# Kernel tuning notes

Hardware: AMD Instinct MI355X
Metric: run time of the kernel (lower is better)

Reference implementation:

```python
import jax, jax.numpy as jnp
import numpy as np

NUM_CLASSES = 10
BIN_STEP = 0.1
N_SAMPLES = 2_000_000
NUM_BINS = 10  # len(arange(0,1.1,0.1)) - 1


def setup_inputs() -> dict:
    key = jax.random.key(0)
    k1, k2 = jax.random.split(key)
    # scaled logits -> softmax so that all confidence bins (incl. (0.9,1.0]) are populated
    logits = jax.random.normal(k1, (N_SAMPLES, NUM_CLASSES), dtype=jnp.float32) * 3.0
    probs = jax.nn.softmax(logits, axis=-1)
    labels = jax.random.randint(k2, (N_SAMPLES,), 0, NUM_CLASSES)
    return {"probs": probs, "labels": labels}


def reference(probs, labels):
    # probs: [N, C] float, labels: [N] int
    n, c = probs.shape
    pred_class = jnp.argmax(probs, axis=1)                      # [N]
    flat = probs.reshape(-1)                                    # [N*C] expanded_preds
    pred_oh = jax.nn.one_hot(pred_class, c, dtype=probs.dtype).reshape(-1)
    tgt_oh = jax.nn.one_hot(labels, c, dtype=probs.dtype).reshape(-1)
    # 1 exactly at the true-class slot of correctly-predicted samples
    correct_vec = tgt_oh * (pred_oh == tgt_oh).astype(probs.dtype)  # [N*C]

    bins = jnp.asarray(np.arange(0.0, 1.1, BIN_STEP), dtype=probs.dtype)  # 11 edges
    # np.digitize(..., right=True) - 1 ; entries exactly 0.0 get idx=-1 and are
    # dropped from every bin, matching the original per-bin masking loop.
    bin_idx = jnp.digitize(flat, bins, right=True) - 1          # [N*C] in [-1, 9]

    zeros = jnp.zeros((NUM_BINS,), dtype=probs.dtype)
    ones = jnp.ones_like(flat)
    # fused single-pass histogram: counts, correct-sums, confidence-sums
    bin_counts = zeros.at[bin_idx].add(ones, mode='drop')
    bin_corrects = zeros.at[bin_idx].add(correct_vec, mode='drop')
    bin_conf_sum = zeros.at[bin_idx].add(flat, mode='drop')

    bin_confidence = bin_conf_sum / bin_counts                  # per-bin mean conf
    bin_acc = bin_corrects / bin_counts                         # per-bin accuracy
    total = jnp.sum(bin_counts)
    ece = jnp.sum(jnp.abs(bin_confidence - bin_acc) * bin_counts) / total

    bin_centers = bins[1:] - BIN_STEP / 2
    return (ece, bin_centers, bin_acc)
```

## Files before the change

### kernel.cpp

```cpp
#include <hip/hip_runtime.h>

#define NBINS 10
#define C 10

constexpr int BLOCK = 256;
constexpr int GRIDH = 1536;
constexpr int GRIDA = 512;
constexpr int PSTR  = 32;


__global__ __launch_bounds__(BLOCK) void ece_fused(
    const float4* __restrict__ p4,
    const int2*   __restrict__ l2,
    float*        __restrict__ part,
    int npairs, int nf4)
{
    __shared__ float        s_red[8 * NBINS];
    __shared__ unsigned int s_cor[NBINS];

    const int tid  = threadIdx.x;
    const int lane = tid & 63, wave = tid >> 6;

    const float EDGE[NBINS] = {
        (float)(0*0.1), (float)(1*0.1), (float)(2*0.1), (float)(3*0.1), (float)(4*0.1),
        (float)(5*0.1), (float)(6*0.1), (float)(7*0.1), (float)(8*0.1), (float)(9*0.1)};

    if (blockIdx.x < GRIDH) {
        const int row = blockIdx.x;
        float        conf[NBINS];
        unsigned int cnt1[NBINS];
        unsigned int nf = 0;
#pragma unroll
        for (int t = 0; t < NBINS; ++t) { conf[t] = 0.0f; cnt1[t] = 0u; }

        const int stride = GRIDH * BLOCK;
        int fi = row * BLOCK + tid;

#define PROC_F4(q)                                                          \
        {                                                                   \
            const float e_[4] = {(q).x, (q).y, (q).z, (q).w};               \
            conf[0] += ((q).x + (q).y) + ((q).z + (q).w);                   \
            _Pragma("unroll")                                               \
            for (int j_ = 0; j_ < 4; ++j_) {                                \
                const float x_ = e_[j_];                                    \
                _Pragma("unroll")                                           \
                for (int t_ = 1; t_ < NBINS; ++t_) {                        \
                    const bool g_ = x_ > EDGE[t_];                          \
                    cnt1[t_] += g_ ? 1u : 0u;             \
                    conf[t_] += g_ ? x_ : 0.0f;          \
                }                                                           \
            }                                                               \
        }

        for (; fi + stride < nf4; fi += 2 * stride) {
            const float4 qa = p4[fi];
            const float4 qb = p4[fi + stride];
            PROC_F4(qa);
            PROC_F4(qb);
            nf += 2;
        }
        if (fi < nf4) {
            const float4 qa = p4[fi];
            PROC_F4(qa);
            nf += 1;
        }
#undef PROC_F4

        unsigned int cnt0 = 4u * nf;

#pragma unroll
        for (int t = 0; t < NBINS; ++t)
            for (int o = 32; o > 0; o >>= 1)
                conf[t] += __shfl_xor(conf[t], o, 64);
        for (int o = 32; o > 0; o >>= 1) cnt0 += __shfl_xor(cnt0, o, 64);
#pragma unroll
        for (int t = 1; t < NBINS; ++t)
            for (int o = 32; o > 0; o >>= 1)
                cnt1[t] += __shfl_xor(cnt1[t], o, 64);

        if (lane == 0) {
#pragma unroll
            for (int t = 0; t < NBINS; ++t) {
                s_red[wave * NBINS + t]             = conf[t];
                s_red[(4 + wave) * NBINS + t]       = (t == 0) ? (float)cnt0 : (float)cnt1[t];
            }
        }
        __syncthreads();

        if (tid < 12) {
            float fc = 0.0f, fn = 0.0f;
            if (tid < NBINS) {
#pragma unroll
                for (int w = 0; w < 4; ++w) {
                    fc += s_red[w * NBINS + tid];
                    fn += s_red[(4 + w) * NBINS + tid];
                }
            }
            part[(size_t)row * PSTR + tid]                = fc;
            part[(size_t)GRIDH * PSTR + row * PSTR + tid] = fn;
        }
    } else {
        const int row = blockIdx.x - GRIDH;
        if (tid < NBINS) s_cor[tid] = 0u;
        __syncthreads();

        const int stride = GRIDA * BLOCK;
        for (int pr = row * BLOCK + tid; pr < npairs; pr += stride) {
            const float4* rw = p4 + (size_t)pr * 5;
            const float4 q0 = rw[0], q1 = rw[1], q2 = rw[2], q3 = rw[3], q4 = rw[4];
            const int2 lab = l2[pr];

            const float mA = fmaxf(fmaxf(fmaxf(fmaxf(q0.x, q0.y), fmaxf(q0.z, q0.w)),
                                         fmaxf(fmaxf(q1.x, q1.y), fmaxf(q1.z, q1.w))),
                                   fmaxf(q2.x, q2.y));
            float plA = q0.x;
            plA = (lab.x == 1) ? q0.y : plA;
            plA = (lab.x == 2) ? q0.z : plA;
            plA = (lab.x == 3) ? q0.w : plA;
            plA = (lab.x == 4) ? q1.x : plA;
            plA = (lab.x == 5) ? q1.y : plA;
            plA = (lab.x == 6) ? q1.z : plA;
            plA = (lab.x == 7) ? q1.w : plA;
            plA = (lab.x == 8) ? q2.x : plA;
            plA = (lab.x == 9) ? q2.y : plA;
            if (plA >= mA) {
                const int im = min((int)ceilf(plA * 10.0f) - 1, NBINS - 1);
                if (im >= 0) atomicAdd(&s_cor[im], 1u);
            }

            const float mB = fmaxf(fmaxf(fmaxf(fmaxf(q2.z, q2.w), fmaxf(q3.x, q3.y)),
                                         fmaxf(fmaxf(q3.z, q3.w), fmaxf(q4.x, q4.y))),
                                   fmaxf(q4.z, q4.w));
            float plB = q2.z;
            plB = (lab.y == 1) ? q2.w : plB;
            plB = (lab.y == 2) ? q3.x : plB;
            plB = (lab.y == 3) ? q3.y : plB;
            plB = (lab.y == 4) ? q3.z : plB;
            plB = (lab.y == 5) ? q3.w : plB;
            plB = (lab.y == 6) ? q4.x : plB;
            plB = (lab.y == 7) ? q4.y : plB;
            plB = (lab.y == 8) ? q4.z : plB;
            plB = (lab.y == 9) ? q4.w : plB;
            if (plB >= mB) {
                const int im = min((int)ceilf(plB * 10.0f) - 1, NBINS - 1);
                if (im >= 0) atomicAdd(&s_cor[im], 1u);
            }
        }
        __syncthreads();

        if (tid < 12) {
            const float v = (tid < NBINS) ? (float)s_cor[tid] : 0.0f;
            part[(size_t)2 * GRIDH * PSTR + row * PSTR + tid] = v;
        }
    }
}

__global__ __launch_bounds__(256) void ece_reduce(
    const float* __restrict__ part,
    float* __restrict__ out)
{
    __shared__ double s_c[4][NBINS];
    __shared__ double s_n[4][NBINS];
    __shared__ double s_r[4][NBINS];

    const int tid = threadIdx.x;
    const int lane = tid & 63, wave = tid >> 6;

    double conf[NBINS], cntd[NBINS], cord[NBINS];
#pragma unroll
    for (int t = 0; t < NBINS; ++t) { conf[t] = 0.0; cntd[t] = 0.0; cord[t] = 0.0; }

    for (int b = tid; b < GRIDH; b += 256) {
        const float4* rc = reinterpret_cast<const float4*>(part + (size_t)b * PSTR);
        const float4* rn = reinterpret_cast<const float4*>(part + (size_t)GRIDH * PSTR + b * PSTR);
        const float4 c0 = rc[0], c1 = rc[1], c2 = rc[2];
        const float4 n0 = rn[0], n1 = rn[1], n2 = rn[2];
        const float cf[12] = {c0.x,c0.y,c0.z,c0.w, c1.x,c1.y,c1.z,c1.w, c2.x,c2.y,c2.z,c2.w};
        const float nf[12] = {n0.x,n0.y,n0.z,n0.w, n1.x,n1.y,n1.z,n1.w, n2.x,n2.y,n2.z,n2.w};
#pragma unroll
        for (int t = 0; t < NBINS; ++t) {
            conf[t] += (double)cf[t];
            cntd[t] += (double)nf[t];
        }
        if (b < GRIDA) {
            const float4* rr = reinterpret_cast<const float4*>(part + (size_t)2 * GRIDH * PSTR + b * PSTR);
            const float4 r0 = rr[0], r1 = rr[1], r2 = rr[2];
            const float rf[12] = {r0.x,r0.y,r0.z,r0.w, r1.x,r1.y,r1.z,r1.w, r2.x,r2.y,r2.z,r2.w};
#pragma unroll
            for (int t = 0; t < NBINS; ++t) cord[t] += (double)rf[t];
        }
    }

#pragma unroll
    for (int t = 0; t < NBINS; ++t) {
        for (int o = 32; o > 0; o >>= 1) {
            conf[t] += __shfl_xor(conf[t], o, 64);
            cntd[t] += __shfl_xor(cntd[t], o, 64);
            cord[t] += __shfl_xor(cord[t], o, 64);
        }
    }
    if (lane == 0) {
#pragma unroll
        for (int t = 0; t < NBINS; ++t) {
            s_c[wave][t] = conf[t]; s_n[wave][t] = cntd[t]; s_r[wave][t] = cord[t];
        }
    }
    __syncthreads();

    if (tid == 0) {
        double S[NBINS + 1], G[NBINS + 1], R[NBINS];
        for (int t = 0; t < NBINS; ++t) {
            G[t] = s_n[0][t] + s_n[1][t] + s_n[2][t] + s_n[3][t];
            R[t] = s_r[0][t] + s_r[1][t] + s_r[2][t] + s_r[3][t];
            S[t] = s_c[0][t] + s_c[1][t] + s_c[2][t] + s_c[3][t];
        }
        S[NBINS] = 0.0; G[NBINS] = 0.0;

        double total = 0.0, ece = 0.0;
        for (int j = 0; j < NBINS; ++j) {
            const double c  = G[j] - G[j + 1];
            const double sc = S[j] - S[j + 1];
            const double ba = R[j] / c;
            total += c;
            ece   += fabs(sc / c - ba) * c;
            out[1 + j]  = (float)((float)((j + 1) * 0.1) - 0.05f);
            out[11 + j] = (float)ba;
        }
        out[0] = (float)(ece / total);
    }
}

extern "C" void kernel_launch(void* const* d_in, const int* in_sizes, int n_in,
                              void* d_out, int out_size, void* d_ws, size_t ws_size,
                              hipStream_t stream)
{
    const float* probs  = (const float*)d_in[0];
    const int*   labels = (const int*)  d_in[1];
    float*       out    = (float*)d_out;
    const int n      = in_sizes[1];
    const int npairs = n / 2;
    const int nf4    = (n * C) / 4;

    float* part = (float*)d_ws;

    ece_fused<<<GRIDH + GRIDA, BLOCK, 0, stream>>>((const float4*)probs,
                                                   (const int2*)labels,
                                                   part, npairs, nf4);
    ece_reduce<<<1, 256, 0, stream>>>(part, out);
}
```

Baseline: 43.45 us.

## Fuse histogram and accuracy passes into a single read of probabilities

Replaces the split grid, where one set of blocks built confidence histograms and another set recomputed argmax/accuracy, with one kernel. Each thread loads a pair of rows once and does both the bin ladder and the correctness counting, so probs is read from memory once instead of twice. The trade-off is more ALU work per thread and strided per-thread row loads instead of fully coalesced float4 streaming. The reduce kernel is updated to read three equally sized partial arrays.

```diff
diff --git a/kernel.cpp b/kernel.cpp
--- a/kernel.cpp
+++ b/kernel.cpp
@@ -4,16 +4,15 @@
 #define C 10
 
 constexpr int BLOCK = 256;
-constexpr int GRIDH = 1536;
-constexpr int GRIDA = 512;
+constexpr int GRID  = 2048;
 constexpr int PSTR  = 32;
 
 
-__global__ __launch_bounds__(BLOCK) void ece_fused(
+__global__ __launch_bounds__(BLOCK) void ece_pass(
     const float4* __restrict__ p4,
     const int2*   __restrict__ l2,
     float*        __restrict__ part,
-    int npairs, int nf4)
+    int npairs)
 {
     __shared__ float        s_red[8 * NBINS];
     __shared__ unsigned int s_cor[NBINS];
@@ -25,133 +24,112 @@
         (float)(0*0.1), (float)(1*0.1), (float)(2*0.1), (float)(3*0.1), (float)(4*0.1),
         (float)(5*0.1), (float)(6*0.1), (float)(7*0.1), (float)(8*0.1), (float)(9*0.1)};
 
-    if (blockIdx.x < GRIDH) {
-        const int row = blockIdx.x;
-        float        conf[NBINS];
-        unsigned int cnt1[NBINS];
-        unsigned int nf = 0;
-#pragma unroll
-        for (int t = 0; t < NBINS; ++t) { conf[t] = 0.0f; cnt1[t] = 0u; }
-
-        const int stride = GRIDH * BLOCK;
-        int fi = row * BLOCK + tid;
-
-#define PROC_F4(q)                                                          \
+    if (tid < NBINS) s_cor[tid] = 0u;
+    __syncthreads();
+
+    float        conf[NBINS];
+    unsigned int cnt1[NBINS];
+    unsigned int np = 0;
+#pragma unroll
+    for (int t = 0; t < NBINS; ++t) { conf[t] = 0.0f; cnt1[t] = 0u; }
+
+#define LADDER(x)                                                           \
         {                                                                   \
-            const float e_[4] = {(q).x, (q).y, (q).z, (q).w};               \
-            conf[0] += ((q).x + (q).y) + ((q).z + (q).w);                   \
             _Pragma("unroll")                                               \
-            for (int j_ = 0; j_ < 4; ++j_) {                                \
-                const float x_ = e_[j_];                                    \
-                _Pragma("unroll")                                           \
-                for (int t_ = 1; t_ < NBINS; ++t_) {                        \
-                    const bool g_ = x_ > EDGE[t_];                          \
-                    cnt1[t_] += g_ ? 1u : 0u;             \
-                    conf[t_] += g_ ? x_ : 0.0f;          \
-                }                                                           \
+            for (int t_ = 1; t_ < NBINS; ++t_) {                            \
+                const bool g_ = (x) > EDGE[t_];                             \
+                cnt1[t_] += g_ ? 1u : 0u;                                   \
+                conf[t_] += g_ ? (x) : 0.0f;                                \
             }                                                               \
         }
 
-        for (; fi + stride < nf4; fi += 2 * stride) {
-            const float4 qa = p4[fi];
-            const float4 qb = p4[fi + stride];
-            PROC_F4(qa);
-            PROC_F4(qb);
-            nf += 2;
-        }
-        if (fi < nf4) {
-            const float4 qa = p4[fi];
-            PROC_F4(qa);
-            nf += 1;
-        }
-#undef PROC_F4
-
-        unsigned int cnt0 = 4u * nf;
-
-#pragma unroll
-        for (int t = 0; t < NBINS; ++t)
-            for (int o = 32; o > 0; o >>= 1)
-                conf[t] += __shfl_xor(conf[t], o, 64);
-        for (int o = 32; o > 0; o >>= 1) cnt0 += __shfl_xor(cnt0, o, 64);
-#pragma unroll
-        for (int t = 1; t < NBINS; ++t)
-            for (int o = 32; o > 0; o >>= 1)
-                cnt1[t] += __shfl_xor(cnt1[t], o, 64);
-
-        if (lane == 0) {
-#pragma unroll
-            for (int t = 0; t < NBINS; ++t) {
-                s_red[wave * NBINS + t]             = conf[t];
-                s_red[(4 + wave) * NBINS + t]       = (t == 0) ? (float)cnt0 : (float)cnt1[t];
+    for (int pr = blockIdx.x * BLOCK + tid; pr < npairs; pr += GRID * BLOCK) {
+        const float4* rw = p4 + (size_t)pr * 5;
+        const float4 q0 = rw[0], q1 = rw[1], q2 = rw[2], q3 = rw[3], q4 = rw[4];
+        const int2 lab = l2[pr];
+        ++np;
+
+        conf[0] += (((q0.x + q0.y) + (q0.z + q0.w)) + ((q1.x + q1.y) + (q1.z + q1.w)))
+                 + (((q2.x + q2.y) + (q2.z + q2.w)) + ((q3.x + q3.y) + (q3.z + q3.w)))
+                 + ((q4.x + q4.y) + (q4.z + q4.w));
+        LADDER(q0.x); LADDER(q0.y); LADDER(q0.z); LADDER(q0.w);
+        LADDER(q1.x); LADDER(q1.y); LADDER(q1.z); LADDER(q1.w);
+        LADDER(q2.x); LADDER(q2.y); LADDER(q2.z); LADDER(q2.w);
+        LADDER(q3.x); LADDER(q3.y); LADDER(q3.z); LADDER(q3.w);
+        LADDER(q4.x); LADDER(q4.y); LADDER(q4.z); LADDER(q4.w);
+
+        const float mA = fmaxf(fmaxf(fmaxf(fmaxf(q0.x, q0.y), fmaxf(q0.z, q0.w)),
+                                     fmaxf(fmaxf(q1.x, q1.y), fmaxf(q1.z, q1.w))),
+                               fmaxf(q2.x, q2.y));
+        float plA = q0.x;
+        plA = (lab.x == 1) ? q0.y : plA;
+        plA = (lab.x == 2) ? q0.z : plA;
+        plA = (lab.x == 3) ? q0.w : plA;
+        plA = (lab.x == 4) ? q1.x : plA;
+        plA = (lab.x == 5) ? q1.y : plA;
+        plA = (lab.x == 6) ? q1.z : plA;
+        plA = (lab.x == 7) ? q1.w : plA;
+        plA = (lab.x == 8) ? q2.x : plA;
+        plA = (lab.x == 9) ? q2.y : plA;
+        if (plA >= mA) {
+            const int im = min((int)ceilf(plA * 10.0f) - 1, NBINS - 1);
+            if (im >= 0) atomicAdd(&s_cor[im], 1u);
+        }
+
+        const float mB = fmaxf(fmaxf(fmaxf(fmaxf(q2.z, q2.w), fmaxf(q3.x, q3.y)),
+                                     fmaxf(fmaxf(q3.z, q3.w), fmaxf(q4.x, q4.y))),
+                               fmaxf(q4.z, q4.w));
+        float plB = q2.z;
+        plB = (lab.y == 1) ? q2.w : plB;
+        plB = (lab.y == 2) ? q3.x : plB;
+        plB = (lab.y == 3) ? q3.y : plB;
+        plB = (lab.y == 4) ? q3.z : plB;
+        plB = (lab.y == 5) ? q3.w : plB;
+        plB = (lab.y == 6) ? q4.x : plB;
+        plB = (lab.y == 7) ? q4.y : plB;
+        plB = (lab.y == 8) ? q4.z : plB;
+        plB = (lab.y == 9) ? q4.w : plB;
+        if (plB >= mB) {
+            const int im = min((int)ceilf(plB * 10.0f) - 1, NBINS - 1);
+            if (im >= 0) atomicAdd(&s_cor[im], 1u);
+        }
+    }
+#undef LADDER
+
+    unsigned int cnt0 = 20u * np;
+
+#pragma unroll
+    for (int t = 0; t < NBINS; ++t)
+        for (int o = 32; o > 0; o >>= 1)
+            conf[t] += __shfl_xor(conf[t], o, 64);
+    for (int o = 32; o > 0; o >>= 1) cnt0 += __shfl_xor(cnt0, o, 64);
+#pragma unroll
+    for (int t = 1; t < NBINS; ++t)
+        for (int o = 32; o > 0; o >>= 1)
+            cnt1[t] += __shfl_xor(cnt1[t], o, 64);
+
+    if (lane == 0) {
+#pragma unroll
+        for (int t = 0; t < NBINS; ++t) {
+            s_red[wave * NBINS + t]       = conf[t];
+            s_red[(4 + wave) * NBINS + t] = (t == 0) ? (float)cnt0 : (float)cnt1[t];
+        }
+    }
+    __syncthreads();
+
+    if (tid < 12) {
+        float fc = 0.0f, fn = 0.0f;
+        if (tid < NBINS) {
+#pragma unroll
+            for (int w = 0; w < 4; ++w) {
+                fc += s_red[w * NBINS + tid];
+                fn += s_red[(4 + w) * NBINS + tid];
             }
         }
-        __syncthreads();
-
-        if (tid < 12) {
-            float fc = 0.0f, fn = 0.0f;
-            if (tid < NBINS) {
-#pragma unroll
-                for (int w = 0; w < 4; ++w) {
-                    fc += s_red[w * NBINS + tid];
-                    fn += s_red[(4 + w) * NBINS + tid];
-                }
-            }
-            part[(size_t)row * PSTR + tid]                = fc;
-            part[(size_t)GRIDH * PSTR + row * PSTR + tid] = fn;
-        }
-    } else {
-        const int row = blockIdx.x - GRIDH;
-        if (tid < NBINS) s_cor[tid] = 0u;
-        __syncthreads();
-
-        const int stride = GRIDA * BLOCK;
-        for (int pr = row * BLOCK + tid; pr < npairs; pr += stride) {
-            const float4* rw = p4 + (size_t)pr * 5;
-            const float4 q0 = rw[0], q1 = rw[1], q2 = rw[2], q3 = rw[3], q4 = rw[4];
-            const int2 lab = l2[pr];
-
-            const float mA = fmaxf(fmaxf(fmaxf(fmaxf(q0.x, q0.y), fmaxf(q0.z, q0.w)),
-                                         fmaxf(fmaxf(q1.x, q1.y), fmaxf(q1.z, q1.w))),
-                                   fmaxf(q2.x, q2.y));
-            float plA = q0.x;
-            plA = (lab.x == 1) ? q0.y : plA;
-            plA = (lab.x == 2) ? q0.z : plA;
-            plA = (lab.x == 3) ? q0.w : plA;
-            plA = (lab.x == 4) ? q1.x : plA;
-            plA = (lab.x == 5) ? q1.y : plA;
-            plA = (lab.x == 6) ? q1.z : plA;
-            plA = (lab.x == 7) ? q1.w : plA;
-            plA = (lab.x == 8) ? q2.x : plA;
-            plA = (lab.x == 9) ? q2.y : plA;
-            if (plA >= mA) {
-                const int im = min((int)ceilf(plA * 10.0f) - 1, NBINS - 1);
-                if (im >= 0) atomicAdd(&s_cor[im], 1u);
-            }
-
-            const float mB = fmaxf(fmaxf(fmaxf(fmaxf(q2.z, q2.w), fmaxf(q3.x, q3.y)),
-                                         fmaxf(fmaxf(q3.z, q3.w), fmaxf(q4.x, q4.y))),
-                                   fmaxf(q4.z, q4.w));
-            float plB = q2.z;
-            plB = (lab.y == 1) ? q2.w : plB;
-            plB = (lab.y == 2) ? q3.x : plB;
-            plB = (lab.y == 3) ? q3.y : plB;
-            plB = (lab.y == 4) ? q3.z : plB;
-            plB = (lab.y == 5) ? q3.w : plB;
-            plB = (lab.y == 6) ? q4.x : plB;
-            plB = (lab.y == 7) ? q4.y : plB;
-            plB = (lab.y == 8) ? q4.z : plB;
-            plB = (lab.y == 9) ? q4.w : plB;
-            if (plB >= mB) {
-                const int im = min((int)ceilf(plB * 10.0f) - 1, NBINS - 1);
-                if (im >= 0) atomicAdd(&s_cor[im], 1u);
-            }
-        }
-        __syncthreads();
-
-        if (tid < 12) {
-            const float v = (tid < NBINS) ? (float)s_cor[tid] : 0.0f;
-            part[(size_t)2 * GRIDH * PSTR + row * PSTR + tid] = v;
-        }
+        const float fr = (tid < NBINS) ? (float)s_cor[tid] : 0.0f;
+        part[(size_t)blockIdx.x * PSTR + tid]                    = fc;
+        part[(size_t)GRID * PSTR + blockIdx.x * PSTR + tid]      = fn;
+        part[(size_t)2 * GRID * PSTR + blockIdx.x * PSTR + tid]  = fr;
     }
 }
 
@@ -170,24 +148,21 @@
 #pragma unroll
     for (int t = 0; t < NBINS; ++t) { conf[t] = 0.0; cntd[t] = 0.0; cord[t] = 0.0; }
 
-    for (int b = tid; b < GRIDH; b += 256) {
+    for (int b = tid; b < GRID; b += 256) {
         const float4* rc = reinterpret_cast<const float4*>(part + (size_t)b * PSTR);
-        const float4* rn = reinterpret_cast<const float4*>(part + (size_t)GRIDH * PSTR + b * PSTR);
+        const float4* rn = reinterpret_cast<const float4*>(part + (size_t)GRID * PSTR + b * PSTR);
+        const float4* rr = reinterpret_cast<const float4*>(part + (size_t)2 * GRID * PSTR + b * PSTR);
         const float4 c0 = rc[0], c1 = rc[1], c2 = rc[2];
         const float4 n0 = rn[0], n1 = rn[1], n2 = rn[2];
+        const float4 r0 = rr[0], r1 = rr[1], r2 = rr[2];
         const float cf[12] = {c0.x,c0.y,c0.z,c0.w, c1.x,c1.y,c1.z,c1.w, c2.x,c2.y,c2.z,c2.w};
         const float nf[12] = {n0.x,n0.y,n0.z,n0.w, n1.x,n1.y,n1.z,n1.w, n2.x,n2.y,n2.z,n2.w};
+        const float rf[12] = {r0.x,r0.y,r0.z,r0.w, r1.x,r1.y,r1.z,r1.w, r2.x,r2.y,r2.z,r2.w};
 #pragma unroll
         for (int t = 0; t < NBINS; ++t) {
             conf[t] += (double)cf[t];
             cntd[t] += (double)nf[t];
-        }
-        if (b < GRIDA) {
-            const float4* rr = reinterpret_cast<const float4*>(part + (size_t)2 * GRIDH * PSTR + b * PSTR);
-            const float4 r0 = rr[0], r1 = rr[1], r2 = rr[2];
-            const float rf[12] = {r0.x,r0.y,r0.z,r0.w, r1.x,r1.y,r1.z,r1.w, r2.x,r2.y,r2.z,r2.w};
-#pragma unroll
-            for (int t = 0; t < NBINS; ++t) cord[t] += (double)rf[t];
+            cord[t] += (double)rf[t];
         }
     }
 
@@ -239,12 +214,10 @@
     float*       out    = (float*)d_out;
     const int n      = in_sizes[1];
     const int npairs = n / 2;
-    const int nf4    = (n * C) / 4;
 
     float* part = (float*)d_ws;
 
-    ece_fused<<<GRIDH + GRIDA, BLOCK, 0, stream>>>((const float4*)probs,
-                                                   (const int2*)labels,
-                                                   part, npairs, nf4);
+    ece_pass<<<GRID, BLOCK, 0, stream>>>((const float4*)probs, (const int2*)labels,
+                                         part, npairs);
     ece_reduce<<<1, 256, 0, stream>>>(part, out);
 }
```

After: 45.55 us. 1.05x slower.
